# Performance work log

Hardware: AMD Instinct MI355X
Metric: run time of the kernel (lower is better)

## Reference

```python
import jax, jax.numpy as jnp
from jax import lax
import numpy as np

B = 8192      # device_size (world_size = 1 -> batch_size == device_size)
D = 512       # projection dim
K = 2048      # number of sampled negatives per anchor
TEMP = 0.5    # temperature
EPS = 1e-8    # torch CosineSimilarity eps


def setup_inputs() -> dict:
    key = jax.random.key(0)
    k1, k2, k3 = jax.random.split(key, 3)
    z_i = jax.random.normal(k1, (B, D), dtype=jnp.float32)
    z_j = jax.random.normal(k2, (B, D), dtype=jnp.float32)
    # neg_perm = torch.randperm(batch_size - 1)[:K]
    neg_perm = jax.random.permutation(k3, B - 1)[:K].astype(jnp.int32)
    return {"z_i": z_i, "z_j": z_j, "neg_perm": neg_perm}


def _logits(z_i, z_j, neg_perm):
    # cosine similarity matrix: (zi . zj) / max(||zi||*||zj||, eps), scaled by 1/T
    ni = jnp.linalg.norm(z_i, axis=1)                       # [B]
    nj = jnp.linalg.norm(z_j, axis=1)                       # [B]
    dots = jnp.einsum('id,jd->ij', z_i, z_j)                # [B,B]
    sim = dots / jnp.maximum(ni[:, None] * nj[None, :], EPS) / TEMP

    pos = jnp.diagonal(sim)                                 # [B] positives
    # row i of sim with diagonal removed has column k -> original column k + (k>=i)
    rows = jnp.arange(B, dtype=neg_perm.dtype)[:, None]     # [B,1]
    cols = neg_perm[None, :] + (neg_perm[None, :] >= rows).astype(neg_perm.dtype)  # [B,K]
    negs = jnp.take_along_axis(sim, cols, axis=1)           # [B,K]
    logits = jnp.concatenate([pos[:, None], negs], axis=1)  # [B,1+K], label = 0
    return logits, pos


def reference(z_i, z_j, neg_perm):
    logits, pos = _logits(z_i, z_j, neg_perm)
    # log(exp(pos) + sum exp(negs)) - pos == logsumexp(logits) - pos
    loss = jnp.sum(jax.nn.logsumexp(logits, axis=1) - pos) / B
    # top-1 / top-5 accuracy against label 0
    _, pred = lax.top_k(logits, 5)                          # [B,5]
    acc1 = jnp.mean((pred[:, 0] == 0).astype(jnp.float32)) * 100.0
    acc5 = jnp.mean(jnp.any(pred == 0, axis=1).astype(jnp.float32)) * 100.0
    return loss, acc1, acc5
```

## Files before the change

### kernel.cpp

```cpp
#include <hip/hip_runtime.h>
#include <cstdint>

#define B_SZ 8192
#define D_SZ 512
#define K_SZ 2048
#define EPSV 1e-8f
#define INV_T 2.0f

typedef float floatx16 __attribute__((ext_vector_type(16)));
typedef int intx8 __attribute__((ext_vector_type(8)));

__device__ __forceinline__ void async_cp16(const void* g, void* l) {
    typedef __attribute__((address_space(1))) unsigned int gds_t;
    typedef __attribute__((address_space(3))) unsigned int lds_t;
    __builtin_amdgcn_global_load_lds((gds_t*)(unsigned long long)g, (lds_t*)l, 16, 0, 0);
}

__device__ __forceinline__ int2 pack_fp8x8(float4 a0, float4 a1) {
    int w0 = __builtin_amdgcn_cvt_pk_fp8_f32(a0.x, a0.y, 0, false);
    w0 = __builtin_amdgcn_cvt_pk_fp8_f32(a0.z, a0.w, w0, true);
    int w1 = __builtin_amdgcn_cvt_pk_fp8_f32(a1.x, a1.y, 0, false);
    w1 = __builtin_amdgcn_cvt_pk_fp8_f32(a1.z, a1.w, w1, true);
    return make_int2(w0, w1);
}

__global__ __launch_bounds__(256) void k_prep(
    const float* __restrict__ zi, const float* __restrict__ zj,
    const int* __restrict__ perm,
    float* __restrict__ ri_arr, float* __restrict__ pos_arr,
    unsigned char* __restrict__ A,
    float4* __restrict__ kmeta, unsigned char* __restrict__ G,
    float* __restrict__ rowacc, float* __restrict__ out)
{
    int w = threadIdx.x >> 6, l = threadIdx.x & 63;
    if (blockIdx.x < 2048) {
        if (blockIdx.x < 64)
            rowacc[blockIdx.x * 256 + threadIdx.x] = 0.f;
        if (blockIdx.x == 0 && threadIdx.x < 3) out[threadIdx.x] = 0.f;
        int row = blockIdx.x * 4 + w;
        const float4* zi4 = (const float4*)(zi + (size_t)row * D_SZ);
        const float4* zj4 = (const float4*)(zj + (size_t)row * D_SZ);
        float4 a0 = zi4[2 * l], a1 = zi4[2 * l + 1];
        float4 b0 = zj4[2 * l], b1 = zj4[2 * l + 1];
        float si = a0.x * a0.x + a0.y * a0.y + a0.z * a0.z + a0.w * a0.w
                 + a1.x * a1.x + a1.y * a1.y + a1.z * a1.z + a1.w * a1.w;
        float sj = b0.x * b0.x + b0.y * b0.y + b0.z * b0.z + b0.w * b0.w
                 + b1.x * b1.x + b1.y * b1.y + b1.z * b1.z + b1.w * b1.w;
        float dd = a0.x * b0.x + a0.y * b0.y + a0.z * b0.z + a0.w * b0.w
                 + a1.x * b1.x + a1.y * b1.y + a1.z * b1.z + a1.w * b1.w;
        for (int m = 1; m < 64; m <<= 1) {
            si += __shfl_xor(si, m);
            sj += __shfl_xor(sj, m);
            dd += __shfl_xor(dd, m);
        }
        if (l == 0) {
            float ni = sqrtf(si), nj = sqrtf(sj);
            ri_arr[row] = INV_T / fmaxf(ni, 1e-6f);
            pos_arr[row] = dd / fmaxf(ni * nj, EPSV) * INV_T;
        }
        *(int2*)(A + (size_t)row * D_SZ + l * 8) = pack_fp8x8(a0, a1);
    } else {
        __shared__ float srj[4];
        int g = (blockIdx.x - 2048) * 4 + w;
        int c0 = perm[g >> 1];
        int c = c0 + (g & 1);
        const float4* src = (const float4*)(zj + (size_t)c * D_SZ);
        float4 a0 = src[2 * l], a1 = src[2 * l + 1];
        float s = a0.x * a0.x + a0.y * a0.y + a0.z * a0.z + a0.w * a0.w
                + a1.x * a1.x + a1.y * a1.y + a1.z * a1.z + a1.w * a1.w;
        for (int m = 1; m < 64; m <<= 1) s += __shfl_xor(s, m);
        if (l == 0) srj[w] = 1.0f / fmaxf(sqrtf(s), 1e-6f);
        __syncthreads();
        if ((w & 1) == 0 && l == 0)
            kmeta[g >> 1] = make_float4(srj[w], srj[w + 1],
                                        __int_as_float(c0), 0.f);
        *(int2*)(G + (size_t)g * D_SZ + l * 8) = pack_fp8x8(a0, a1);
    }
}

__global__ __launch_bounds__(512, 2) void k_gemm(
    const unsigned char* __restrict__ A,
    const unsigned char* __restrict__ G,
    const float4* __restrict__ kmeta,
    const float* __restrict__ ri_arr,
    const float* __restrict__ pos_arr,
    float* __restrict__ rowacc)
{
    __shared__ unsigned char lds[4][2][16384];
    const int tid = threadIdx.x;
    const int l = tid & 63, w = tid >> 6;
    const int wm = w >> 1, wn = w & 1;
    const int ln = l & 31, q = l >> 5;

    const int bid = blockIdx.x;
    const int xcd = bid & 7;
    const int slot = bid >> 3;
    const int gTile = xcd * 2 + (slot & 1);
    const int aTile = slot >> 1;
    const int gBase = gTile * 256;
    const int aBase = aTile * 256;

    size_t aOff[2], gOff[2];
    int ldsOff[2];
    #pragma unroll
    for (int it = 0; it < 2; ++it) {
        int fc = it * 512 + tid;
        int r = fc >> 2, s = fc & 3;
        int scc = s ^ ((r ^ (r >> 2)) & 3);
        aOff[it] = (size_t)(aBase + r) * D_SZ + scc * 16;
        gOff[it] = (size_t)(gBase + r) * D_SZ + scc * 16;
        ldsOff[it] = fc * 16;
    }

#define STAGE(t_) do {                                                      \
        unsigned char* Ad_ = &lds[(t_) & 3][0][0];                          \
        unsigned char* Gd_ = &lds[(t_) & 3][1][0];                          \
        size_t ko_ = (size_t)(t_) * 64;                                     \
        async_cp16(A + aOff[0] + ko_, Ad_ + ldsOff[0]);                     \
        async_cp16(A + aOff[1] + ko_, Ad_ + ldsOff[1]);                     \
        async_cp16(G + gOff[0] + ko_, Gd_ + ldsOff[0]);                     \
        async_cp16(G + gOff[1] + ko_, Gd_ + ldsOff[1]);                     \
    } while (0)

    int aAddr[4][2], gAddr[2][2];
    #pragma unroll
    for (int tn = 0; tn < 4; ++tn) {
        int ar = wn * 128 + tn * 32 + ln;
        int xa = (ar ^ (ar >> 2)) & 3;
        aAddr[tn][0] = ar * 64 + ((2 * q) ^ xa) * 16;
        aAddr[tn][1] = ar * 64 + ((2 * q + 1) ^ xa) * 16;
    }
    #pragma unroll
    for (int tm = 0; tm < 2; ++tm) {
        int gr = wm * 64 + tm * 32 + ln;
        int xg = (gr ^ (gr >> 2)) & 3;
        gAddr[tm][0] = gr * 64 + ((2 * q) ^ xg) * 16;
        gAddr[tm][1] = gr * 64 + ((2 * q + 1) ^ xg) * 16;
    }

    floatx16 acc[2][4] = {};

    STAGE(0); STAGE(1); STAGE(2);

    #pragma unroll 1
    for (int t = 0; t < 8; ++t) {
        if (t < 6)       asm volatile("s_waitcnt vmcnt(8)" ::: "memory");
        else if (t == 6) asm volatile("s_waitcnt vmcnt(4)" ::: "memory");
        else             asm volatile("s_waitcnt vmcnt(0)" ::: "memory");
        __builtin_amdgcn_s_barrier();
        __builtin_amdgcn_sched_barrier(0);
        if (t < 5) STAGE(t + 3);
        const unsigned char* Ab = &lds[t & 3][0][0];
        const unsigned char* Gb = &lds[t & 3][1][0];
        intx8 af[4], gf[2];
        #pragma unroll
        for (int tn = 0; tn < 4; ++tn) {
            int4 lo = *(const int4*)(Ab + aAddr[tn][0]);
            int4 hi = *(const int4*)(Ab + aAddr[tn][1]);
            af[tn][0] = lo.x; af[tn][1] = lo.y; af[tn][2] = lo.z; af[tn][3] = lo.w;
            af[tn][4] = hi.x; af[tn][5] = hi.y; af[tn][6] = hi.z; af[tn][7] = hi.w;
        }
        #pragma unroll
        for (int tm = 0; tm < 2; ++tm) {
            int4 lo = *(const int4*)(Gb + gAddr[tm][0]);
            int4 hi = *(const int4*)(Gb + gAddr[tm][1]);
            gf[tm][0] = lo.x; gf[tm][1] = lo.y; gf[tm][2] = lo.z; gf[tm][3] = lo.w;
            gf[tm][4] = hi.x; gf[tm][5] = hi.y; gf[tm][6] = hi.z; gf[tm][7] = hi.w;
        }
        __builtin_amdgcn_s_setprio(1);
        #pragma unroll
        for (int tm = 0; tm < 2; ++tm)
            #pragma unroll
            for (int tn = 0; tn < 4; ++tn)
                acc[tm][tn] = __builtin_amdgcn_mfma_scale_f32_32x32x64_f8f6f4(
                    gf[tm], af[tn], acc[tm][tn],
                    0, 0,
                    0, 0x7f7f7f7f,
                    0, 0x7f7f7f7f);
        __builtin_amdgcn_s_setprio(0);
    }
#undef STAGE

    int anc[4]; float riv[4], pv[4];
    float pe[4] = {0.f, 0.f, 0.f, 0.f}, pc[4] = {0.f, 0.f, 0.f, 0.f};
    #pragma unroll
    for (int tn = 0; tn < 4; ++tn) {
        anc[tn] = aBase + wn * 128 + tn * 32 + ln;
        riv[tn] = ri_arr[anc[tn]];
        pv[tn] = pos_arr[anc[tn]];
    }
    #pragma unroll
    for (int tm = 0; tm < 2; ++tm) {
        #pragma unroll
        for (int j = 0; j < 4; ++j) {
            int k0 = gTile * 128 + wm * 32 + tm * 16 + 4 * j + 2 * q;
            float4 m0 = kmeta[k0];
            float4 m1 = kmeta[k0 + 1];
            #pragma unroll
            for (int p = 0; p < 2; ++p) {
                float4 md = p ? m1 : m0;
                int c0 = __float_as_int(md.z);
                int re = 4 * j + 2 * p;
                #pragma unroll
                for (int tn = 0; tn < 4; ++tn) {
                    bool sel = (c0 >= anc[tn]);
                    float v = sel ? acc[tm][tn][re + 1] : acc[tm][tn][re];
                    float rj = sel ? md.y : md.x;
                    float logit = v * riv[tn] * rj;
                    pe[tn] += __expf(logit);
                    pc[tn] += (logit > pv[tn]) ? 1.f : 0.f;
                }
            }
        }
    }
    #pragma unroll
    for (int tn = 0; tn < 4; ++tn) {
        pe[tn] += __shfl_xor(pe[tn], 32);
        pc[tn] += __shfl_xor(pc[tn], 32);
        if (q == 0) {
            atomicAdd(&rowacc[anc[tn]], pe[tn]);
            atomicAdd(&rowacc[B_SZ + anc[tn]], pc[tn]);
        }
    }
}

__global__ __launch_bounds__(256) void k_final(
    const float* __restrict__ rowacc, const float* __restrict__ pos_arr,
    float* __restrict__ out)
{
    int row = blockIdx.x * 256 + threadIdx.x;
    float pe = rowacc[row];
    float pc = rowacc[B_SZ + row];
    float pos = pos_arr[row];
    float loss = logf(__expf(pos) + pe) - pos;
    float a1 = (pc < 0.5f) ? 1.f : 0.f;
    float a5 = (pc < 4.5f) ? 1.f : 0.f;
    for (int m = 1; m < 64; m <<= 1) {
        loss += __shfl_xor(loss, m);
        a1 += __shfl_xor(a1, m);
        a5 += __shfl_xor(a5, m);
    }
    __shared__ float red[3][4];
    int w = threadIdx.x >> 6, l = threadIdx.x & 63;
    if (l == 0) { red[0][w] = loss; red[1][w] = a1; red[2][w] = a5; }
    __syncthreads();
    if (threadIdx.x == 0) {
        float L = red[0][0] + red[0][1] + red[0][2] + red[0][3];
        float A1 = red[1][0] + red[1][1] + red[1][2] + red[1][3];
        float A5 = red[2][0] + red[2][1] + red[2][2] + red[2][3];
        atomicAdd(&out[0], L / (float)B_SZ);
        atomicAdd(&out[1], A1 * (100.f / (float)B_SZ));
        atomicAdd(&out[2], A5 * (100.f / (float)B_SZ));
    }
}

extern "C" void kernel_launch(void* const* d_in, const int* in_sizes, int n_in,
                              void* d_out, int out_size, void* d_ws, size_t ws_size,
                              hipStream_t stream)
{
    const float* zi = (const float*)d_in[0];
    const float* zj = (const float*)d_in[1];
    const int* perm = (const int*)d_in[2];
    float* out = (float*)d_out;

    char* p = (char*)d_ws;
    unsigned char* A = (unsigned char*)p;    p += (size_t)B_SZ * D_SZ;
    unsigned char* G = (unsigned char*)p;    p += (size_t)2 * K_SZ * D_SZ;
    float* ri_arr = (float*)p;               p += (size_t)B_SZ * 4;
    float* pos_arr = (float*)p;              p += (size_t)B_SZ * 4;
    float4* kmeta = (float4*)p;              p += (size_t)K_SZ * 16;
    float* rowacc = (float*)p;               p += (size_t)2 * B_SZ * 4;

    k_prep<<<2048 + 1024, 256, 0, stream>>>(zi, zj, perm, ri_arr, pos_arr, A,
                                            kmeta, G, rowacc, out);
    k_gemm<<<512, 512, 0, stream>>>(A, G, kmeta, ri_arr, pos_arr, rowacc);
    k_final<<<32, 256, 0, stream>>>(rowacc, pos_arr, out);
}
```

Measured before the change: 52.07 us.

## Split A/G async loads and interleave them with MFMA halves in main loop

Splits each stage's global-to-LDS copy into separate A and G halves. These are issued between the two halves of the MFMA work in each K step, with extra barriers and waitcnts moved to the end of the iteration. The aim is to overlap memory issue with compute more finely and spread VMEM traffic across the loop. In exchange it adds two more workgroup barriers per iteration and needs careful vmcnt accounting to stay correct.

```diff
diff --git a/kernel.cpp b/kernel.cpp
--- a/kernel.cpp
+++ b/kernel.cpp
@@ -112,12 +112,15 @@
         ldsOff[it] = fc * 16;
     }
 
-#define STAGE(t_) do {                                                      \
+#define STAGE_A(t_) do {                                                    \
         unsigned char* Ad_ = &lds[(t_) & 3][0][0];                          \
-        unsigned char* Gd_ = &lds[(t_) & 3][1][0];                          \
         size_t ko_ = (size_t)(t_) * 64;                                     \
         async_cp16(A + aOff[0] + ko_, Ad_ + ldsOff[0]);                     \
         async_cp16(A + aOff[1] + ko_, Ad_ + ldsOff[1]);                     \
+    } while (0)
+#define STAGE_G(t_) do {                                                    \
+        unsigned char* Gd_ = &lds[(t_) & 3][1][0];                          \
+        size_t ko_ = (size_t)(t_) * 64;                                     \
         async_cp16(G + gOff[0] + ko_, Gd_ + ldsOff[0]);                     \
         async_cp16(G + gOff[1] + ko_, Gd_ + ldsOff[1]);                     \
     } while (0)
@@ -140,16 +143,16 @@
 
     floatx16 acc[2][4] = {};
 
-    STAGE(0); STAGE(1); STAGE(2);
+    STAGE_A(0); STAGE_G(0);
+    STAGE_A(1); STAGE_G(1);
+    STAGE_A(2); STAGE_G(2);
+    asm volatile("s_waitcnt vmcnt(8)" ::: "memory");
+    __builtin_amdgcn_sched_barrier(0);
+    __builtin_amdgcn_s_barrier();
+    __builtin_amdgcn_sched_barrier(0);
 
     #pragma unroll 1
     for (int t = 0; t < 8; ++t) {
-        if (t < 6)       asm volatile("s_waitcnt vmcnt(8)" ::: "memory");
-        else if (t == 6) asm volatile("s_waitcnt vmcnt(4)" ::: "memory");
-        else             asm volatile("s_waitcnt vmcnt(0)" ::: "memory");
-        __builtin_amdgcn_s_barrier();
-        __builtin_amdgcn_sched_barrier(0);
-        if (t < 5) STAGE(t + 3);
         const unsigned char* Ab = &lds[t & 3][0][0];
         const unsigned char* Gb = &lds[t & 3][1][0];
         intx8 af[4], gf[2];
@@ -167,19 +170,37 @@
             gf[tm][0] = lo.x; gf[tm][1] = lo.y; gf[tm][2] = lo.z; gf[tm][3] = lo.w;
             gf[tm][4] = hi.x; gf[tm][5] = hi.y; gf[tm][6] = hi.z; gf[tm][7] = hi.w;
         }
+        if (t < 5) STAGE_A(t + 3);
+        __builtin_amdgcn_sched_barrier(0);
+        __builtin_amdgcn_s_barrier();
+        __builtin_amdgcn_sched_barrier(0);
         __builtin_amdgcn_s_setprio(1);
         #pragma unroll
-        for (int tm = 0; tm < 2; ++tm)
-            #pragma unroll
-            for (int tn = 0; tn < 4; ++tn)
-                acc[tm][tn] = __builtin_amdgcn_mfma_scale_f32_32x32x64_f8f6f4(
-                    gf[tm], af[tn], acc[tm][tn],
-                    0, 0,
-                    0, 0x7f7f7f7f,
-                    0, 0x7f7f7f7f);
+        for (int tn = 0; tn < 4; ++tn)
+            acc[0][tn] = __builtin_amdgcn_mfma_scale_f32_32x32x64_f8f6f4(
+                gf[0], af[tn], acc[0][tn],
+                0, 0, 0, 0x7f7f7f7f, 0, 0x7f7f7f7f);
         __builtin_amdgcn_s_setprio(0);
-    }
-#undef STAGE
+        if (t < 5) STAGE_G(t + 3);
+        __builtin_amdgcn_sched_barrier(0);
+        __builtin_amdgcn_s_barrier();
+        __builtin_amdgcn_sched_barrier(0);
+        __builtin_amdgcn_s_setprio(1);
+        #pragma unroll
+        for (int tn = 0; tn < 4; ++tn)
+            acc[1][tn] = __builtin_amdgcn_mfma_scale_f32_32x32x64_f8f6f4(
+                gf[1], af[tn], acc[1][tn],
+                0, 0, 0, 0x7f7f7f7f, 0, 0x7f7f7f7f);
+        __builtin_amdgcn_s_setprio(0);
+        if (t < 5)       asm volatile("s_waitcnt vmcnt(8)" ::: "memory");
+        else if (t == 5) asm volatile("s_waitcnt vmcnt(4)" ::: "memory");
+        else if (t == 6) asm volatile("s_waitcnt vmcnt(0)" ::: "memory");
+        __builtin_amdgcn_sched_barrier(0);
+        __builtin_amdgcn_s_barrier();
+        __builtin_amdgcn_sched_barrier(0);
+    }
+#undef STAGE_A
+#undef STAGE_G
 
     int anc[4]; float riv[4], pv[4];
     float pe[4] = {0.f, 0.f, 0.f, 0.f}, pc[4] = {0.f, 0.f, 0.f, 0.f};
```

Result: no change. 52.05 us (-0.0%).
